# Kernel tuning notes

Hardware: AMD Instinct MI355X
Metric: run time of the kernel (lower is better)

Reference implementation:

```python
import jax, jax.numpy as jnp
import numpy as np

N = 500000      # active voxels
C_IN = 16       # input voxel feature dim
# encoder channels per stage: 32, 64, 128


def setup_inputs() -> dict:
    key = jax.random.key(0)
    ks = jax.random.split(key, 16)

    def w(k, i, o):
        return jax.random.normal(k, (i, o), dtype=jnp.float32) * (1.0 / np.sqrt(i))

    d = {}
    d['feat'] = jax.random.normal(ks[0], (N, C_IN), dtype=jnp.float32)
    d['coords'] = jax.random.randint(ks[1], (N, 4), 0, 1024, dtype=jnp.int32)
    d['W_in'] = w(ks[2], C_IN, 32)
    d['W_enc1'] = w(ks[3], 32, 32)
    d['W_enc2'] = w(ks[4], 32, 64)
    d['W_enc3'] = w(ks[5], 64, 128)
    d['W_lat1'] = w(ks[6], 32, 32)
    d['W_lat2'] = w(ks[7], 64, 64)
    d['W_lat3'] = w(ks[8], 128, 128)
    d['W_merge1'] = w(ks[9], 64, 32)    # merge: 2*C_i -> C_i
    d['W_merge2'] = w(ks[10], 128, 64)
    d['W_merge3'] = w(ks[11], 256, 128)
    d['W_up1'] = w(ks[12], 32, 32)      # upsample: C_i -> C_{i-1}
    d['W_up2'] = w(ks[13], 64, 32)
    d['W_up3'] = w(ks[14], 128, 64)
    return d


def _forward(feat, W_in, W_enc1, W_enc2, W_enc3, W_lat1, W_lat2, W_lat3,
             W_merge1, W_merge2, W_merge3, W_up1, W_up2, W_up3):
    relu = jax.nn.relu
    # conv_input + encoder (1x1 submanifold sparse convs == per-voxel matmul)
    x = relu(feat @ W_in)
    e1 = relu(x @ W_enc1)
    e2 = relu(e1 @ W_enc2)
    e3 = relu(e2 @ W_enc3)
    enc = [e1, e2, e3]
    lats = [W_lat1, W_lat2, W_lat3]
    mrgs = [W_merge1, W_merge2, W_merge3]
    ups = [W_up1, W_up2, W_up3]
    x = e3
    for i in (2, 1, 0):  # decoder stages stage_num..1
        lat = relu(enc[i] @ lats[i])                    # lateral_layer
        # cat0(x_bottom) + cat1(lat): identity-placement 1x1 convs == concat
        cat = jnp.concatenate([x, lat], axis=-1)        # [N, 2*C_i]
        merge = relu(cat @ mrgs[i])                     # merge_layer 2C->C
        red = cat.reshape(cat.shape[0], -1, 2).sum(-1)  # reduce_channel: fixed pairwise-sum conv
        x = relu((merge + red) @ ups[i])                # residual add + upsample_layer
    return x  # ret['voxel_feats']


def reference(feat, coords, W_in, W_enc1, W_enc2, W_enc3, W_lat1, W_lat2, W_lat3,
              W_merge1, W_merge2, W_merge3, W_up1, W_up2, W_up3):
    # coords define sparse structure; for 1x1 subm convs the math only touches features
    return _forward(feat, W_in, W_enc1, W_enc2, W_enc3, W_lat1, W_lat2, W_lat3,
                    W_merge1, W_merge2, W_merge3, W_up1, W_up2, W_up3)
```

## Files before the change

kernel.cpp:

```cpp
#include <hip/hip_runtime.h>

typedef unsigned short u16;
typedef _Float16 h16;
typedef __attribute__((ext_vector_type(8))) _Float16 half8;
typedef __attribute__((ext_vector_type(8))) unsigned short ushort8;
typedef __attribute__((ext_vector_type(4))) float f32x4;

#define N_STRIPS 31250
#define NPAIRS   15625
#define STRIP    16384

#define MFMA16(A,B,C) __builtin_amdgcn_mfma_f32_16x16x32_f16(A,B,C,0,0,0)

#define LBAR() asm volatile("s_waitcnt lgkmcnt(0)\n\ts_barrier" ::: "memory")

#define F_L0   0
#define F_L1   2
#define F_L2   4
#define F_L3   8
#define F_L4   24
#define F_L5   56
#define F_L6   120
#define F_L7   136
#define F_L8   144
#define F_L9   160
#define F_L10  164
#define F_L11  166
#define F_L12  170
#define NFRAG  172

__device__ __forceinline__ u16 hb(h16 h) { union { h16 h; u16 u; } v; v.h = h; return v.u; }

__global__ __launch_bounds__(256) void pack_w(
    const float* w0, const float* w1, const float* w2, const float* w3, const float* w4,
    const float* w5, const float* w6, const float* w7, const float* w8, const float* w9,
    const float* w10, const float* w11, const float* w12, u16* __restrict__ packed)
{
  const float* ws[13] = {w0,w1,w2,w3,w4,w5,w6,w7,w8,w9,w10,w11,w12};
  const int Ka[13]  = {16,32,32,64,128,256,128,64,128,64,32,64,32};
  const int KT[13]  = {1,1,1,2,4,8,4,2,4,2,1,2,1};
  const int CO[13]  = {32,32,64,128,128,128,64,64,64,32,32,32,32};
  const int FO[13]  = {F_L0,F_L1,F_L2,F_L3,F_L4,F_L5,F_L6,F_L7,F_L8,F_L9,F_L10,F_L11,F_L12};
  int g = blockIdx.x * 256 + threadIdx.x;
  int f = g >> 6, lane = g & 63;
  if (f >= NFRAG) return;
  int layer = 0;
#pragma unroll
  for (int i = 1; i < 13; ++i) if (f >= FO[i]) layer = i;
  int fl = f - FO[layer];
  int kt = fl % KT[layer];
  int ct = fl / KT[layer];
  int cout = CO[layer];
  int quad = lane >> 4;
  int col  = ct * 16 + (lane & 15);
  u16 thi[8], tlo[8];
#pragma unroll
  for (int j = 0; j < 8; ++j) {
    int k = kt * 32 + quad * 8 + j;
    float w = (k < Ka[layer]) ? ws[layer][k * cout + col] : 0.f;
    h16 h = (h16)w;
    h16 l = (h16)(w - (float)h);
    thi[j] = hb(h); tlo[j] = hb(l);
  }
  u16* dst = packed + ((size_t)f * 64 + lane) * 16;
  *(ushort8*)dst       = *(const ushort8*)thi;
  *(ushort8*)(dst + 8) = *(const ushort8*)tlo;
}


__device__ __forceinline__ void splitw(h16* dst, int idx, int lo, float v) {
  h16 h = (h16)v;
  dst[idx]      = h;
  dst[idx + lo] = (h16)(v - (float)h);
}
__device__ __forceinline__ float red4(const h16* cat, int cs, int rr, int cc) {
  const h16* p = cat + rr * cs + 2 * cc;
  const h16* q = p + 16 * cs;
  return (float)p[0] + (float)p[1] + (float)q[0] + (float)q[1];
}

template<int EPI>
__device__ __forceinline__ void epilogue(
    f32x4 a0, f32x4 a1, int ct, int lane,
    h16* dst, int ds, int colb, const h16* cat, int cs,
    float* __restrict__ gout, int row0)
{
  const int l15 = lane & 15, quad = lane >> 4;
  const int dlo = 16 * ds;
#pragma unroll
  for (int r = 0; r < 4; ++r) {
    const int rr = quad * 4 + r;
    const int cc = ct * 16 + l15;
    float v0 = a0[r] > 0.f ? a0[r] : 0.f;
    float v1 = a1[r] > 0.f ? a1[r] : 0.f;
    if (EPI == 1) {
      v0 += red4(cat, cs, rr, cc);
      v1 += red4(cat + STRIP, cs, rr, cc);
    }
    if (EPI <= 1) {
      splitw(dst,         rr * ds + colb + cc, dlo, v0);
      splitw(dst + STRIP, rr * ds + colb + cc, dlo, v1);
    } else {
      gout[(size_t)(row0 + rr) * 32 + cc]      = v0;
      gout[(size_t)(row0 + 16 + rr) * 32 + cc] = v1;
    }
  }
}

template<int KT, int EPI>
__device__ __forceinline__ void layerW(
    const h16* __restrict__ asrc, int as,
    const h16* __restrict__ wp, int foff, int ct, int lane,
    half8 pbh, half8 pbl,
    h16* dst, int ds, int colb, const h16* cat, int cs,
    float* __restrict__ gout, int row0)
{
  const int l15 = lane & 15, quad = lane >> 4;
  const int abase = l15 * as + quad * 8;
  const int alo = 16 * as;
  f32x4 a0 = {0.f,0.f,0.f,0.f}, a1 = {0.f,0.f,0.f,0.f};
#pragma unroll
  for (int kt = 0; kt < KT; ++kt) {
    half8 bhv, blv;
    if (kt == 0) { bhv = pbh; blv = pbl; }
    else {
      const h16* fp = wp + (((size_t)(foff + ct * KT + kt)) * 64 + lane) * 16;
      bhv = *(const half8*)fp;
      blv = *(const half8*)(fp + 8);
    }
    half8 ah0 = *(const half8*)(asrc + abase + kt * 32);
    half8 al0 = *(const half8*)(asrc + alo + abase + kt * 32);
    half8 ah1 = *(const half8*)(asrc + STRIP + abase + kt * 32);
    half8 al1 = *(const half8*)(asrc + STRIP + alo + abase + kt * 32);
    a0 = MFMA16(al0, bhv, a0); a0 = MFMA16(ah0, blv, a0); a0 = MFMA16(ah0, bhv, a0);
    a1 = MFMA16(al1, bhv, a1); a1 = MFMA16(ah1, blv, a1); a1 = MFMA16(ah1, bhv, a1);
  }
  epilogue<EPI>(a0, a1, ct, lane, dst, ds, colb, cat, cs, gout, row0);
}

#define PFB(FOFF, CT_, KT_)                                                       \
  do { const h16* _fp = wp + (((size_t)((FOFF) + (CT_) * (KT_))) * 64 + lane) * 16; \
       pbh = *(const half8*)_fp; pbl = *(const half8*)(_fp + 8); } while (0)

__global__ __launch_bounds__(512, 4) void backbone(
    const float* __restrict__ feat, const h16* __restrict__ wp, float* __restrict__ out)
{
  __shared__ h16 lds[2 * STRIP];
  const int lane = threadIdx.x & 63;
  const int wv   = threadIdx.x >> 6;
  const int l15 = lane & 15, quad = lane >> 4;
  const int row0 = blockIdx.x * 32;

  h16* E1 = lds;            const int SE1 = 40;
  h16* E2 = lds + 1280;     const int SE2 = 72;
  h16* CT = lds + 3584;     const int SCT = 264;
  h16* MR = lds + 12032;    const int SMR = 136;

  half8 pbh, pbl;

  if (wv < 2) {
    PFB(F_L0, wv, 1);
    h16 th0[8] = {0,0,0,0,0,0,0,0}, tl0[8] = {0,0,0,0,0,0,0,0};
    h16 th1[8] = {0,0,0,0,0,0,0,0}, tl1[8] = {0,0,0,0,0,0,0,0};
    if (quad < 2) {
      const float* s0 = feat + (size_t)(row0 + l15) * 16 + quad * 8;
      const float* s1 = feat + (size_t)(row0 + 16 + l15) * 16 + quad * 8;
#pragma unroll
      for (int j = 0; j < 8; ++j) {
        float v0 = s0[j], v1 = s1[j];
        h16 h0 = (h16)v0, h1 = (h16)v1;
        th0[j] = h0; tl0[j] = (h16)(v0 - (float)h0);
        th1[j] = h1; tl1[j] = (h16)(v1 - (float)h1);
      }
    }
    half8 ah0 = *(const half8*)th0, al0 = *(const half8*)tl0;
    half8 ah1 = *(const half8*)th1, al1 = *(const half8*)tl1;
    f32x4 a0 = {0.f,0.f,0.f,0.f}, a1 = {0.f,0.f,0.f,0.f};
    a0 = MFMA16(al0, pbh, a0); a0 = MFMA16(ah0, pbl, a0); a0 = MFMA16(ah0, pbh, a0);
    a1 = MFMA16(al1, pbh, a1); a1 = MFMA16(ah1, pbl, a1); a1 = MFMA16(ah1, pbh, a1);
    epilogue<0>(a0, a1, wv, lane, CT, SCT, 0, nullptr, 0, nullptr, 0);
    PFB(F_L1, wv, 1);
  }
  LBAR();

  if (wv < 2) {
    layerW<1,0>(CT,SCT, wp, F_L1, wv, lane, pbh,pbl, E1,SE1,0, nullptr,0, nullptr,0);
  }
  if (wv < 4) PFB(F_L2, wv, 1);
  LBAR();

  if (wv < 4) {
    layerW<1,0>(E1,SE1, wp, F_L2, wv, lane, pbh,pbl, E2,SE2,0, nullptr,0, nullptr,0);
  }
  PFB(F_L3, wv, 2);
  LBAR();

  layerW<2,0>(E2,SE2, wp, F_L3, wv, lane, pbh,pbl, CT,SCT,0, nullptr,0, nullptr,0);
  PFB(F_L4, wv, 4);
  LBAR();

  layerW<4,0>(CT,SCT, wp, F_L4, wv, lane, pbh,pbl, CT,SCT,128, nullptr,0, nullptr,0);
  PFB(F_L5, wv, 8);
  LBAR();

  layerW<8,1>(CT,SCT, wp, F_L5, wv, lane, pbh,pbl, MR,SMR,0, CT,SCT, nullptr,0);
  if (wv < 4) PFB(F_L6, wv, 4); else PFB(F_L7, wv - 4, 2);
  LBAR();

  if (wv < 4) {
    layerW<4,0>(MR,SMR, wp, F_L6, wv, lane, pbh,pbl, CT,SCT,0,  nullptr,0, nullptr,0);
  } else {
    layerW<2,0>(E2,SE2, wp, F_L7, wv - 4, lane, pbh,pbl, CT,SCT,64, nullptr,0, nullptr,0);
  }
  if (wv < 4) PFB(F_L8, wv, 4);
  LBAR();

  if (wv < 4) {
    layerW<4,1>(CT,SCT, wp, F_L8, wv, lane, pbh,pbl, MR,SMR,0, CT,SCT, nullptr,0);
  }
  if (wv < 2) PFB(F_L9, wv, 2);
  else if (wv < 4) PFB(F_L10, wv - 2, 1);
  LBAR();

  if (wv < 2) {
    layerW<2,0>(MR,SMR, wp, F_L9, wv, lane, pbh,pbl, CT,SCT,0,  nullptr,0, nullptr,0);
  } else if (wv < 4) {
    layerW<1,0>(E1,SE1, wp, F_L10, wv - 2, lane, pbh,pbl, CT,SCT,32, nullptr,0, nullptr,0);
  }
  if (wv < 2) PFB(F_L11, wv, 2);
  LBAR();

  if (wv < 2) {
    layerW<2,1>(CT,SCT, wp, F_L11, wv, lane, pbh,pbl, MR,SMR,0, CT,SCT, nullptr,0);
    PFB(F_L12, wv, 1);
  }
  LBAR();

  if (wv < 2) {
    layerW<1,2>(MR,SMR, wp, F_L12, wv, lane, pbh,pbl, nullptr,0,0, nullptr,0, out, row0);
  }
}

extern "C" void kernel_launch(void* const* d_in, const int* in_sizes, int n_in,
                              void* d_out, int out_size, void* d_ws, size_t ws_size,
                              hipStream_t stream) {
  (void)in_sizes; (void)n_in; (void)out_size; (void)ws_size;
  u16* packed = (u16*)d_ws;

  hipLaunchKernelGGL(pack_w, dim3(43), dim3(256), 0, stream,
      (const float*)d_in[2],  (const float*)d_in[3],  (const float*)d_in[4],
      (const float*)d_in[5],  (const float*)d_in[8],  (const float*)d_in[11],
      (const float*)d_in[14], (const float*)d_in[7],  (const float*)d_in[10],
      (const float*)d_in[13], (const float*)d_in[6],  (const float*)d_in[9],
      (const float*)d_in[12], packed);

  hipLaunchKernelGGL(backbone, dim3(NPAIRS), dim3(512), 0, stream,
                     (const float*)d_in[0], (const h16*)packed, (float*)d_out);
}
```

Measured before the change: 452.5 us.

## Process four 16-row strips per block with multi-tile waves to reuse weights

Each block now handles 64 voxels (four strips) in 128KB of dynamic LDS instead of 32, and waves are remapped so that each computes several column tiles and/or strips. Every weight fragment loaded from global memory is then reused across more MFMAs, and all 8 waves stay busy in the narrow layers instead of idling. The feature load is vectorised and a bounds check handles the tail block. In exchange, LDS per block grows fourfold and occupancy drops to two blocks per CU, while register pressure rises from the multi-accumulator tiles.

```diff
diff --git a/kernel.cpp b/kernel.cpp
--- a/kernel.cpp
+++ b/kernel.cpp
@@ -3,12 +3,22 @@
 typedef unsigned short u16;
 typedef _Float16 h16;
 typedef __attribute__((ext_vector_type(8))) _Float16 half8;
+typedef __attribute__((ext_vector_type(2))) _Float16 half2v;
 typedef __attribute__((ext_vector_type(8))) unsigned short ushort8;
 typedef __attribute__((ext_vector_type(4))) float f32x4;
 
-#define N_STRIPS 31250
-#define NPAIRS   15625
-#define STRIP    16384
+#define NVOX  500000
+#define NBLK  7813
+#define STRIP 16384
+
+#define AE1 0
+#define SE1 40
+#define AE2 1280
+#define SE2 72
+#define ACT 3584
+#define SCT 264
+#define AMR 12032
+#define SMR 136
 
 #define MFMA16(A,B,C) __builtin_amdgcn_mfma_f32_16x16x32_f16(A,B,C,0,0,0)
 
@@ -68,177 +78,192 @@
 }
 
 
-__device__ __forceinline__ void splitw(h16* dst, int idx, int lo, float v) {
-  h16 h = (h16)v;
-  dst[idx]      = h;
-  dst[idx + lo] = (h16)(v - (float)h);
-}
-__device__ __forceinline__ float red4(const h16* cat, int cs, int rr, int cc) {
-  const h16* p = cat + rr * cs + 2 * cc;
-  const h16* q = p + 16 * cs;
-  return (float)p[0] + (float)p[1] + (float)q[0] + (float)q[1];
-}
-
-template<int EPI>
-__device__ __forceinline__ void epilogue(
-    f32x4 a0, f32x4 a1, int ct, int lane,
-    h16* dst, int ds, int colb, const h16* cat, int cs,
+__device__ __forceinline__ float red2(const h16* p) {
+  half2v v = *reinterpret_cast<const half2v*>(p);
+  return (float)v.x + (float)v.y;
+}
+
+template<int KT, int NCT, int CTS, int NSP, int EPI>
+__device__ __forceinline__ void unitW(
+    h16* __restrict__ lds, int s0, int aoff, int as,
+    const h16* __restrict__ wp, int foff, int c0, int lane,
+    half8 pbh, half8 pbl,
+    int doff, int ds, int colb, int catoff, int cs,
     float* __restrict__ gout, int row0)
 {
   const int l15 = lane & 15, quad = lane >> 4;
-  const int dlo = 16 * ds;
-#pragma unroll
-  for (int r = 0; r < 4; ++r) {
-    const int rr = quad * 4 + r;
-    const int cc = ct * 16 + l15;
-    float v0 = a0[r] > 0.f ? a0[r] : 0.f;
-    float v1 = a1[r] > 0.f ? a1[r] : 0.f;
-    if (EPI == 1) {
-      v0 += red4(cat, cs, rr, cc);
-      v1 += red4(cat + STRIP, cs, rr, cc);
-    }
+  const int abase = aoff + l15 * as + quad * 8;
+  f32x4 acc[NSP][NCT];
+#pragma unroll
+  for (int sp = 0; sp < NSP; ++sp)
+#pragma unroll
+    for (int i = 0; i < NCT; ++i) acc[sp][i] = (f32x4){0.f,0.f,0.f,0.f};
+
+#pragma unroll
+  for (int kt = 0; kt < KT; ++kt) {
+    half8 bh[NCT], bl[NCT];
+#pragma unroll
+    for (int i = 0; i < NCT; ++i) {
+      if (kt == 0 && i == 0) { bh[0] = pbh; bl[0] = pbl; }
+      else {
+        const h16* fp = wp + (((size_t)(foff + (c0 + i * CTS) * KT + kt)) * 64 + lane) * 16;
+        bh[i] = *(const half8*)fp;
+        bl[i] = *(const half8*)(fp + 8);
+      }
+    }
+#pragma unroll
+    for (int sp = 0; sp < NSP; ++sp) {
+      const h16* ab = lds + (s0 + sp) * STRIP + abase + kt * 32;
+      half8 ah = *(const half8*)ab;
+      half8 al = *(const half8*)(ab + 16 * as);
+#pragma unroll
+      for (int i = 0; i < NCT; ++i) {
+        acc[sp][i] = MFMA16(al, bh[i], acc[sp][i]);
+        acc[sp][i] = MFMA16(ah, bl[i], acc[sp][i]);
+        acc[sp][i] = MFMA16(ah, bh[i], acc[sp][i]);
+      }
+    }
+  }
+
+#pragma unroll
+  for (int sp = 0; sp < NSP; ++sp) {
     if (EPI <= 1) {
-      splitw(dst,         rr * ds + colb + cc, dlo, v0);
-      splitw(dst + STRIP, rr * ds + colb + cc, dlo, v1);
+      h16* dstS = lds + (s0 + sp) * STRIP + doff;
+      const h16* catS = lds + (s0 + sp) * STRIP + catoff;
+      const int dlo = 16 * ds;
+#pragma unroll
+      for (int i = 0; i < NCT; ++i) {
+        const int cc = (c0 + i * CTS) * 16 + l15;
+#pragma unroll
+        for (int r = 0; r < 4; ++r) {
+          const int rr = quad * 4 + r;
+          float v = acc[sp][i][r];
+          v = v > 0.f ? v : 0.f;
+          if (EPI == 1)
+            v += red2(catS + rr * cs + 2 * cc) + red2(catS + (rr + 16) * cs + 2 * cc);
+          const int idx = rr * ds + colb + cc;
+          h16 h = (h16)v;
+          dstS[idx]       = h;
+          dstS[idx + dlo] = (h16)(v - (float)h);
+        }
+      }
     } else {
-      gout[(size_t)(row0 + rr) * 32 + cc]      = v0;
-      gout[(size_t)(row0 + 16 + rr) * 32 + cc] = v1;
-    }
-  }
-}
-
-template<int KT, int EPI>
-__device__ __forceinline__ void layerW(
-    const h16* __restrict__ asrc, int as,
-    const h16* __restrict__ wp, int foff, int ct, int lane,
-    half8 pbh, half8 pbl,
-    h16* dst, int ds, int colb, const h16* cat, int cs,
-    float* __restrict__ gout, int row0)
-{
-  const int l15 = lane & 15, quad = lane >> 4;
-  const int abase = l15 * as + quad * 8;
-  const int alo = 16 * as;
-  f32x4 a0 = {0.f,0.f,0.f,0.f}, a1 = {0.f,0.f,0.f,0.f};
-#pragma unroll
-  for (int kt = 0; kt < KT; ++kt) {
-    half8 bhv, blv;
-    if (kt == 0) { bhv = pbh; blv = pbl; }
-    else {
-      const h16* fp = wp + (((size_t)(foff + ct * KT + kt)) * 64 + lane) * 16;
-      bhv = *(const half8*)fp;
-      blv = *(const half8*)(fp + 8);
-    }
-    half8 ah0 = *(const half8*)(asrc + abase + kt * 32);
-    half8 al0 = *(const half8*)(asrc + alo + abase + kt * 32);
-    half8 ah1 = *(const half8*)(asrc + STRIP + abase + kt * 32);
-    half8 al1 = *(const half8*)(asrc + STRIP + alo + abase + kt * 32);
-    a0 = MFMA16(al0, bhv, a0); a0 = MFMA16(ah0, blv, a0); a0 = MFMA16(ah0, bhv, a0);
-    a1 = MFMA16(al1, bhv, a1); a1 = MFMA16(ah1, blv, a1); a1 = MFMA16(ah1, bhv, a1);
-  }
-  epilogue<EPI>(a0, a1, ct, lane, dst, ds, colb, cat, cs, gout, row0);
-}
-
-#define PFB(FOFF, CT_, KT_)                                                       \
-  do { const h16* _fp = wp + (((size_t)((FOFF) + (CT_) * (KT_))) * 64 + lane) * 16; \
+      const int gr0 = row0 + (s0 + sp) * 16;
+#pragma unroll
+      for (int i = 0; i < NCT; ++i) {
+        const int cc = (c0 + i * CTS) * 16 + l15;
+#pragma unroll
+        for (int r = 0; r < 4; ++r) {
+          const int rr = quad * 4 + r;
+          float v = acc[sp][i][r];
+          v = v > 0.f ? v : 0.f;
+          const int grow = gr0 + rr;
+          if (grow < NVOX) gout[(size_t)grow * 32 + cc] = v;
+        }
+      }
+    }
+  }
+}
+
+#define PFB(FOFF, CIDX, KT_)                                                        \
+  do { const h16* _fp = wp + (((size_t)((FOFF) + (CIDX) * (KT_))) * 64 + lane) * 16; \
        pbh = *(const half8*)_fp; pbl = *(const half8*)(_fp + 8); } while (0)
-
-__global__ __launch_bounds__(512, 4) void backbone(
+#define PFB2(FOFF, CIDX, KT_)                                                       \
+  do { const h16* _fp = wp + (((size_t)((FOFF) + (CIDX) * (KT_))) * 64 + lane) * 16; \
+       pbh2 = *(const half8*)_fp; pbl2 = *(const half8*)(_fp + 8); } while (0)
+
+__global__ __launch_bounds__(512, 2) void backbone(
     const float* __restrict__ feat, const h16* __restrict__ wp, float* __restrict__ out)
 {
-  __shared__ h16 lds[2 * STRIP];
+  extern __shared__ h16 lds[];
   const int lane = threadIdx.x & 63;
   const int wv   = threadIdx.x >> 6;
   const int l15 = lane & 15, quad = lane >> 4;
-  const int row0 = blockIdx.x * 32;
-
-  h16* E1 = lds;            const int SE1 = 40;
-  h16* E2 = lds + 1280;     const int SE2 = 72;
-  h16* CT = lds + 3584;     const int SCT = 264;
-  h16* MR = lds + 12032;    const int SMR = 136;
-
-  half8 pbh, pbl;
-
-  if (wv < 2) {
-    PFB(F_L0, wv, 1);
-    h16 th0[8] = {0,0,0,0,0,0,0,0}, tl0[8] = {0,0,0,0,0,0,0,0};
-    h16 th1[8] = {0,0,0,0,0,0,0,0}, tl1[8] = {0,0,0,0,0,0,0,0};
-    if (quad < 2) {
-      const float* s0 = feat + (size_t)(row0 + l15) * 16 + quad * 8;
-      const float* s1 = feat + (size_t)(row0 + 16 + l15) * 16 + quad * 8;
-#pragma unroll
-      for (int j = 0; j < 8; ++j) {
-        float v0 = s0[j], v1 = s1[j];
-        h16 h0 = (h16)v0, h1 = (h16)v1;
-        th0[j] = h0; tl0[j] = (h16)(v0 - (float)h0);
-        th1[j] = h1; tl1[j] = (h16)(v1 - (float)h1);
-      }
-    }
-    half8 ah0 = *(const half8*)th0, al0 = *(const half8*)tl0;
-    half8 ah1 = *(const half8*)th1, al1 = *(const half8*)tl1;
-    f32x4 a0 = {0.f,0.f,0.f,0.f}, a1 = {0.f,0.f,0.f,0.f};
-    a0 = MFMA16(al0, pbh, a0); a0 = MFMA16(ah0, pbl, a0); a0 = MFMA16(ah0, pbh, a0);
-    a1 = MFMA16(al1, pbh, a1); a1 = MFMA16(ah1, pbl, a1); a1 = MFMA16(ah1, pbh, a1);
-    epilogue<0>(a0, a1, wv, lane, CT, SCT, 0, nullptr, 0, nullptr, 0);
-    PFB(F_L1, wv, 1);
-  }
-  LBAR();
-
-  if (wv < 2) {
-    layerW<1,0>(CT,SCT, wp, F_L1, wv, lane, pbh,pbl, E1,SE1,0, nullptr,0, nullptr,0);
-  }
-  if (wv < 4) PFB(F_L2, wv, 1);
-  LBAR();
-
-  if (wv < 4) {
-    layerW<1,0>(E1,SE1, wp, F_L2, wv, lane, pbh,pbl, E2,SE2,0, nullptr,0, nullptr,0);
-  }
-  PFB(F_L3, wv, 2);
-  LBAR();
-
-  layerW<2,0>(E2,SE2, wp, F_L3, wv, lane, pbh,pbl, CT,SCT,0, nullptr,0, nullptr,0);
-  PFB(F_L4, wv, 4);
-  LBAR();
-
-  layerW<4,0>(CT,SCT, wp, F_L4, wv, lane, pbh,pbl, CT,SCT,128, nullptr,0, nullptr,0);
-  PFB(F_L5, wv, 8);
-  LBAR();
-
-  layerW<8,1>(CT,SCT, wp, F_L5, wv, lane, pbh,pbl, MR,SMR,0, CT,SCT, nullptr,0);
-  if (wv < 4) PFB(F_L6, wv, 4); else PFB(F_L7, wv - 4, 2);
-  LBAR();
-
-  if (wv < 4) {
-    layerW<4,0>(MR,SMR, wp, F_L6, wv, lane, pbh,pbl, CT,SCT,0,  nullptr,0, nullptr,0);
-  } else {
-    layerW<2,0>(E2,SE2, wp, F_L7, wv - 4, lane, pbh,pbl, CT,SCT,64, nullptr,0, nullptr,0);
-  }
-  if (wv < 4) PFB(F_L8, wv, 4);
-  LBAR();
-
-  if (wv < 4) {
-    layerW<4,1>(CT,SCT, wp, F_L8, wv, lane, pbh,pbl, MR,SMR,0, CT,SCT, nullptr,0);
-  }
-  if (wv < 2) PFB(F_L9, wv, 2);
-  else if (wv < 4) PFB(F_L10, wv - 2, 1);
-  LBAR();
-
-  if (wv < 2) {
-    layerW<2,0>(MR,SMR, wp, F_L9, wv, lane, pbh,pbl, CT,SCT,0,  nullptr,0, nullptr,0);
-  } else if (wv < 4) {
-    layerW<1,0>(E1,SE1, wp, F_L10, wv - 2, lane, pbh,pbl, CT,SCT,32, nullptr,0, nullptr,0);
-  }
-  if (wv < 2) PFB(F_L11, wv, 2);
-  LBAR();
-
-  if (wv < 2) {
-    layerW<2,1>(CT,SCT, wp, F_L11, wv, lane, pbh,pbl, MR,SMR,0, CT,SCT, nullptr,0);
-    PFB(F_L12, wv, 1);
-  }
-  LBAR();
-
-  if (wv < 2) {
-    layerW<1,2>(MR,SMR, wp, F_L12, wv, lane, pbh,pbl, nullptr,0,0, nullptr,0, out, row0);
-  }
+  const int row0 = blockIdx.x * 64;
+
+  const int sA = wv & 3;
+  const int cA = wv >> 2;
+  const int cB = wv & 3;
+  const int sB = (wv >> 2) * 2;
+
+  half8 pbh, pbl, pbh2, pbl2;
+
+  PFB(F_L0, cA, 1);
+  {
+    const int grow = row0 + sA * 16 + l15;
+    half8 ah = {0,0,0,0,0,0,0,0}, al = {0,0,0,0,0,0,0,0};
+    if (quad < 2 && grow < NVOX) {
+      const float* s = feat + (size_t)grow * 16 + quad * 8;
+      f32x4 u0 = *(const f32x4*)s;
+      f32x4 u1 = *(const f32x4*)(s + 4);
+      h16 th[8], tl[8];
+#pragma unroll
+      for (int j = 0; j < 4; ++j) {
+        h16 h = (h16)u0[j]; th[j] = h; tl[j] = (h16)(u0[j] - (float)h);
+      }
+#pragma unroll
+      for (int j = 0; j < 4; ++j) {
+        h16 h = (h16)u1[j]; th[4+j] = h; tl[4+j] = (h16)(u1[j] - (float)h);
+      }
+      ah = *(const half8*)th; al = *(const half8*)tl;
+    }
+    f32x4 a = {0.f,0.f,0.f,0.f};
+    a = MFMA16(al, pbh, a); a = MFMA16(ah, pbl, a); a = MFMA16(ah, pbh, a);
+    h16* dstS = lds + sA * STRIP + ACT;
+#pragma unroll
+    for (int r = 0; r < 4; ++r) {
+      const int rr = quad * 4 + r;
+      float v = a[r] > 0.f ? a[r] : 0.f;
+      const int idx = rr * SCT + cA * 16 + l15;
+      h16 h = (h16)v;
+      dstS[idx]            = h;
+      dstS[idx + 16 * SCT] = (h16)(v - (float)h);
+    }
+  }
+  PFB(F_L1, cA, 1);
+  LBAR();
+
+  unitW<1,1,1,1,0>(lds, sA, ACT, SCT, wp, F_L1, cA, lane, pbh, pbl, AE1, SE1, 0, 0, 0, nullptr, 0);
+  PFB(F_L2, cA, 1);
+  LBAR();
+
+  unitW<1,2,2,1,0>(lds, sA, AE1, SE1, wp, F_L2, cA, lane, pbh, pbl, AE2, SE2, 0, 0, 0, nullptr, 0);
+  PFB(F_L3, cB, 2);
+  LBAR();
+
+  unitW<2,2,4,2,0>(lds, sB, AE2, SE2, wp, F_L3, cB, lane, pbh, pbl, ACT, SCT, 0, 0, 0, nullptr, 0);
+  PFB(F_L4, cB, 4);
+  LBAR();
+
+  unitW<4,2,4,2,0>(lds, sB, ACT, SCT, wp, F_L4, cB, lane, pbh, pbl, ACT, SCT, 128, 0, 0, nullptr, 0);
+  PFB(F_L5, cB, 8);
+  LBAR();
+
+  unitW<8,2,4,2,1>(lds, sB, ACT, SCT, wp, F_L5, cB, lane, pbh, pbl, AMR, SMR, 0, ACT, SCT, nullptr, 0);
+  PFB (F_L6, cA, 4);
+  PFB2(F_L7, cA, 2);
+  LBAR();
+
+  unitW<4,2,2,1,0>(lds, sA, AMR, SMR, wp, F_L6, cA, lane, pbh,  pbl,  ACT, SCT, 0,  0, 0, nullptr, 0);
+  unitW<2,2,2,1,0>(lds, sA, AE2, SE2, wp, F_L7, cA, lane, pbh2, pbl2, ACT, SCT, 64, 0, 0, nullptr, 0);
+  PFB(F_L8, cA, 4);
+  LBAR();
+
+  unitW<4,2,2,1,1>(lds, sA, ACT, SCT, wp, F_L8, cA, lane, pbh, pbl, AMR, SMR, 0, ACT, SCT, nullptr, 0);
+  PFB (F_L9,  cA, 2);
+  PFB2(F_L10, cA, 1);
+  LBAR();
+
+  unitW<2,1,1,1,0>(lds, sA, AMR, SMR, wp, F_L9,  cA, lane, pbh,  pbl,  ACT, SCT, 0,  0, 0, nullptr, 0);
+  unitW<1,1,1,1,0>(lds, sA, AE1, SE1, wp, F_L10, cA, lane, pbh2, pbl2, ACT, SCT, 32, 0, 0, nullptr, 0);
+  PFB(F_L11, cA, 2);
+  LBAR();
+
+  unitW<2,1,1,1,1>(lds, sA, ACT, SCT, wp, F_L11, cA, lane, pbh, pbl, AMR, SMR, 0, ACT, SCT, nullptr, 0);
+  PFB(F_L12, cA, 1);
+  LBAR();
+
+  unitW<1,1,1,1,2>(lds, sA, AMR, SMR, wp, F_L12, cA, lane, pbh, pbl, 0, 0, 0, 0, 0, out, row0);
 }
 
 extern "C" void kernel_launch(void* const* d_in, const int* in_sizes, int n_in,
@@ -246,6 +271,13 @@
                               hipStream_t stream) {
   (void)in_sizes; (void)n_in; (void)out_size; (void)ws_size;
   u16* packed = (u16*)d_ws;
+
+  static bool att_set = false;
+  if (!att_set) {
+    hipFuncSetAttribute((const void*)backbone,
+                        hipFuncAttributeMaxDynamicSharedMemorySize, 131072);
+    att_set = true;
+  }
 
   hipLaunchKernelGGL(pack_w, dim3(43), dim3(256), 0, stream,
       (const float*)d_in[2],  (const float*)d_in[3],  (const float*)d_in[4],
@@ -254,6 +286,6 @@
       (const float*)d_in[13], (const float*)d_in[6],  (const float*)d_in[9],
       (const float*)d_in[12], packed);
 
-  hipLaunchKernelGGL(backbone, dim3(NPAIRS), dim3(512), 0, stream,
+  hipLaunchKernelGGL(backbone, dim3(NBLK), dim3(512), 131072, stream,
                      (const float*)d_in[0], (const h16*)packed, (float*)d_out);
 }
```

Result: slower. 504.4 us (+11.5%).

## Interleave hi/lo fp16 pairs in LDS and alias merge buffer to shrink shared memory

Applied to the files above, without the earlier changes.

Activations in LDS are now stored with each value's hi and lo fp16 halves interleaved in one 32-bit word, replacing separate hi and lo planes. The MR buffer now overlaps CT, made safe by an extra barrier inside the layer-5 epilogue, which is placed after the reads of CT and before the writes. Together these shrink per-block LDS so the launch bound can rise to 6 blocks per CU. Operand loads now need shuffles to de-interleave, and the input load is vectorized. The intent is higher occupancy and fewer LDS store instructions, at the cost of extra shuffle ALU work and a possibly more fragile buffer-aliasing schedule.

```diff
diff --git a/kernel.cpp b/kernel.cpp
--- a/kernel.cpp
+++ b/kernel.cpp
@@ -1,14 +1,24 @@
 #include <hip/hip_runtime.h>
 
 typedef unsigned short u16;
+typedef unsigned int u32;
 typedef _Float16 h16;
+typedef __attribute__((ext_vector_type(4))) _Float16 half4;
 typedef __attribute__((ext_vector_type(8))) _Float16 half8;
 typedef __attribute__((ext_vector_type(8))) unsigned short ushort8;
 typedef __attribute__((ext_vector_type(4))) float f32x4;
 
-#define N_STRIPS 31250
-#define NPAIRS   15625
-#define STRIP    16384
+#define NPAIRS 15625
+#define STRIPO 11648
+
+#define AE1 0
+#define SE1 72
+#define AE2 1152
+#define SE2 136
+#define ACT 3328
+#define SCT 520
+#define AMR 3584
+#define SMR 520
 
 #define MFMA16(A,B,C) __builtin_amdgcn_mfma_f32_16x16x32_f16(A,B,C,0,0,0)
 
@@ -68,46 +78,20 @@
 }
 
 
-__device__ __forceinline__ void splitw(h16* dst, int idx, int lo, float v) {
+__device__ __forceinline__ void packw(h16* dst, int idx2, float v) {
   h16 h = (h16)v;
-  dst[idx]      = h;
-  dst[idx + lo] = (h16)(v - (float)h);
-}
-__device__ __forceinline__ float red4(const h16* cat, int cs, int rr, int cc) {
-  const h16* p = cat + rr * cs + 2 * cc;
-  const h16* q = p + 16 * cs;
-  return (float)p[0] + (float)p[1] + (float)q[0] + (float)q[1];
-}
-
-template<int EPI>
-__device__ __forceinline__ void epilogue(
-    f32x4 a0, f32x4 a1, int ct, int lane,
-    h16* dst, int ds, int colb, const h16* cat, int cs,
-    float* __restrict__ gout, int row0)
-{
-  const int l15 = lane & 15, quad = lane >> 4;
-  const int dlo = 16 * ds;
-#pragma unroll
-  for (int r = 0; r < 4; ++r) {
-    const int rr = quad * 4 + r;
-    const int cc = ct * 16 + l15;
-    float v0 = a0[r] > 0.f ? a0[r] : 0.f;
-    float v1 = a1[r] > 0.f ? a1[r] : 0.f;
-    if (EPI == 1) {
-      v0 += red4(cat, cs, rr, cc);
-      v1 += red4(cat + STRIP, cs, rr, cc);
-    }
-    if (EPI <= 1) {
-      splitw(dst,         rr * ds + colb + cc, dlo, v0);
-      splitw(dst + STRIP, rr * ds + colb + cc, dlo, v1);
-    } else {
-      gout[(size_t)(row0 + rr) * 32 + cc]      = v0;
-      gout[(size_t)(row0 + 16 + rr) * 32 + cc] = v1;
-    }
-  }
-}
-
-template<int KT, int EPI>
+  h16 l = (h16)(v - (float)h);
+  union { u16 s[2]; u32 u; } z;
+  z.s[0] = hb(h); z.s[1] = hb(l);
+  *reinterpret_cast<u32*>(dst + idx2) = z.u;
+}
+
+__device__ __forceinline__ float red2i(const h16* cat, int cs, int rr, int cc) {
+  half4 v = *reinterpret_cast<const half4*>(cat + rr * cs + 4 * cc);
+  return (float)v.x + (float)v.y + (float)v.z + (float)v.w;
+}
+
+template<int KT, int EPI, int BAR>
 __device__ __forceinline__ void layerW(
     const h16* __restrict__ asrc, int as,
     const h16* __restrict__ wp, int foff, int ct, int lane,
@@ -116,8 +100,7 @@
     float* __restrict__ gout, int row0)
 {
   const int l15 = lane & 15, quad = lane >> 4;
-  const int abase = l15 * as + quad * 8;
-  const int alo = 16 * as;
+  const int abase = l15 * as + quad * 16;
   f32x4 a0 = {0.f,0.f,0.f,0.f}, a1 = {0.f,0.f,0.f,0.f};
 #pragma unroll
   for (int kt = 0; kt < KT; ++kt) {
@@ -128,33 +111,66 @@
       bhv = *(const half8*)fp;
       blv = *(const half8*)(fp + 8);
     }
-    half8 ah0 = *(const half8*)(asrc + abase + kt * 32);
-    half8 al0 = *(const half8*)(asrc + alo + abase + kt * 32);
-    half8 ah1 = *(const half8*)(asrc + STRIP + abase + kt * 32);
-    half8 al1 = *(const half8*)(asrc + STRIP + alo + abase + kt * 32);
+    const h16* p0 = asrc + abase + kt * 64;
+    const h16* p1 = p0 + STRIPO;
+    half8 q0a = *(const half8*)p0, q0b = *(const half8*)(p0 + 8);
+    half8 q1a = *(const half8*)p1, q1b = *(const half8*)(p1 + 8);
+    half8 ah0 = __builtin_shufflevector(q0a, q0b, 0,2,4,6,8,10,12,14);
+    half8 al0 = __builtin_shufflevector(q0a, q0b, 1,3,5,7,9,11,13,15);
+    half8 ah1 = __builtin_shufflevector(q1a, q1b, 0,2,4,6,8,10,12,14);
+    half8 al1 = __builtin_shufflevector(q1a, q1b, 1,3,5,7,9,11,13,15);
     a0 = MFMA16(al0, bhv, a0); a0 = MFMA16(ah0, blv, a0); a0 = MFMA16(ah0, bhv, a0);
     a1 = MFMA16(al1, bhv, a1); a1 = MFMA16(ah1, blv, a1); a1 = MFMA16(ah1, bhv, a1);
   }
-  epilogue<EPI>(a0, a1, ct, lane, dst, ds, colb, cat, cs, gout, row0);
-}
-
-#define PFB(FOFF, CT_, KT_)                                                       \
-  do { const h16* _fp = wp + (((size_t)((FOFF) + (CT_) * (KT_))) * 64 + lane) * 16; \
+  const int cc = ct * 16 + l15;
+  float v0r[4], v1r[4];
+#pragma unroll
+  for (int r = 0; r < 4; ++r) {
+    const int rr = quad * 4 + r;
+    float v0 = a0[r] > 0.f ? a0[r] : 0.f;
+    float v1 = a1[r] > 0.f ? a1[r] : 0.f;
+    if (EPI == 1) {
+      v0 += red2i(cat, cs, rr, cc);
+      v1 += red2i(cat + STRIPO, cs, rr, cc);
+    }
+    v0r[r] = v0; v1r[r] = v1;
+  }
+  if (BAR) LBAR();
+  if (EPI <= 1) {
+#pragma unroll
+    for (int r = 0; r < 4; ++r) {
+      const int rr = quad * 4 + r;
+      const int idx2 = rr * ds + 2 * (colb + cc);
+      packw(dst, idx2, v0r[r]);
+      packw(dst + STRIPO, idx2, v1r[r]);
+    }
+  } else {
+#pragma unroll
+    for (int r = 0; r < 4; ++r) {
+      const int rr = quad * 4 + r;
+      gout[(size_t)(row0 + rr) * 32 + cc]      = v0r[r];
+      gout[(size_t)(row0 + 16 + rr) * 32 + cc] = v1r[r];
+    }
+  }
+}
+
+#define PFB(FOFF, CIDX, KT_)                                                        \
+  do { const h16* _fp = wp + (((size_t)((FOFF) + (CIDX) * (KT_))) * 64 + lane) * 16; \
        pbh = *(const half8*)_fp; pbl = *(const half8*)(_fp + 8); } while (0)
 
-__global__ __launch_bounds__(512, 4) void backbone(
+__global__ __launch_bounds__(512, 6) void backbone(
     const float* __restrict__ feat, const h16* __restrict__ wp, float* __restrict__ out)
 {
-  __shared__ h16 lds[2 * STRIP];
+  __shared__ h16 lds[2 * STRIPO];
   const int lane = threadIdx.x & 63;
   const int wv   = threadIdx.x >> 6;
   const int l15 = lane & 15, quad = lane >> 4;
   const int row0 = blockIdx.x * 32;
 
-  h16* E1 = lds;            const int SE1 = 40;
-  h16* E2 = lds + 1280;     const int SE2 = 72;
-  h16* CT = lds + 3584;     const int SCT = 264;
-  h16* MR = lds + 12032;    const int SMR = 136;
+  h16* E1 = lds + AE1;
+  h16* E2 = lds + AE2;
+  h16* CT = lds + ACT;
+  h16* MR = lds + AMR;
 
   half8 pbh, pbl;
 
@@ -165,12 +181,15 @@
     if (quad < 2) {
       const float* s0 = feat + (size_t)(row0 + l15) * 16 + quad * 8;
       const float* s1 = feat + (size_t)(row0 + 16 + l15) * 16 + quad * 8;
-#pragma unroll
-      for (int j = 0; j < 8; ++j) {
-        float v0 = s0[j], v1 = s1[j];
-        h16 h0 = (h16)v0, h1 = (h16)v1;
-        th0[j] = h0; tl0[j] = (h16)(v0 - (float)h0);
-        th1[j] = h1; tl1[j] = (h16)(v1 - (float)h1);
+      f32x4 u0a = *(const f32x4*)s0, u0b = *(const f32x4*)(s0 + 4);
+      f32x4 u1a = *(const f32x4*)s1, u1b = *(const f32x4*)(s1 + 4);
+#pragma unroll
+      for (int j = 0; j < 4; ++j) {
+        h16 h;
+        h = (h16)u0a[j]; th0[j]   = h; tl0[j]   = (h16)(u0a[j] - (float)h);
+        h = (h16)u0b[j]; th0[4+j] = h; tl0[4+j] = (h16)(u0b[j] - (float)h);
+        h = (h16)u1a[j]; th1[j]   = h; tl1[j]   = (h16)(u1a[j] - (float)h);
+        h = (h16)u1b[j]; th1[4+j] = h; tl1[4+j] = (h16)(u1b[j] - (float)h);
       }
     }
     half8 ah0 = *(const half8*)th0, al0 = *(const half8*)tl0;
@@ -178,66 +197,72 @@
     f32x4 a0 = {0.f,0.f,0.f,0.f}, a1 = {0.f,0.f,0.f,0.f};
     a0 = MFMA16(al0, pbh, a0); a0 = MFMA16(ah0, pbl, a0); a0 = MFMA16(ah0, pbh, a0);
     a1 = MFMA16(al1, pbh, a1); a1 = MFMA16(ah1, pbl, a1); a1 = MFMA16(ah1, pbh, a1);
-    epilogue<0>(a0, a1, wv, lane, CT, SCT, 0, nullptr, 0, nullptr, 0);
+#pragma unroll
+    for (int r = 0; r < 4; ++r) {
+      const int rr = quad * 4 + r;
+      const int idx2 = rr * SCT + 2 * (wv * 16 + l15);
+      packw(CT,          idx2, a0[r] > 0.f ? a0[r] : 0.f);
+      packw(CT + STRIPO, idx2, a1[r] > 0.f ? a1[r] : 0.f);
+    }
     PFB(F_L1, wv, 1);
   }
   LBAR();
 
   if (wv < 2) {
-    layerW<1,0>(CT,SCT, wp, F_L1, wv, lane, pbh,pbl, E1,SE1,0, nullptr,0, nullptr,0);
+    layerW<1,0,0>(CT,SCT, wp, F_L1, wv, lane, pbh,pbl, E1,SE1,0, nullptr,0, nullptr,0);
   }
   if (wv < 4) PFB(F_L2, wv, 1);
   LBAR();
 
   if (wv < 4) {
-    layerW<1,0>(E1,SE1, wp, F_L2, wv, lane, pbh,pbl, E2,SE2,0, nullptr,0, nullptr,0);
+    layerW<1,0,0>(E1,SE1, wp, F_L2, wv, lane, pbh,pbl, E2,SE2,0, nullptr,0, nullptr,0);
   }
   PFB(F_L3, wv, 2);
   LBAR();
 
-  layerW<2,0>(E2,SE2, wp, F_L3, wv, lane, pbh,pbl, CT,SCT,0, nullptr,0, nullptr,0);
+  layerW<2,0,0>(E2,SE2, wp, F_L3, wv, lane, pbh,pbl, CT,SCT,0, nullptr,0, nullptr,0);
   PFB(F_L4, wv, 4);
   LBAR();
 
-  layerW<4,0>(CT,SCT, wp, F_L4, wv, lane, pbh,pbl, CT,SCT,128, nullptr,0, nullptr,0);
+  layerW<4,0,0>(CT,SCT, wp, F_L4, wv, lane, pbh,pbl, CT,SCT,128, nullptr,0, nullptr,0);
   PFB(F_L5, wv, 8);
   LBAR();
 
-  layerW<8,1>(CT,SCT, wp, F_L5, wv, lane, pbh,pbl, MR,SMR,0, CT,SCT, nullptr,0);
+  layerW<8,1,1>(CT,SCT, wp, F_L5, wv, lane, pbh,pbl, MR,SMR,0, CT,SCT, nullptr,0);
   if (wv < 4) PFB(F_L6, wv, 4); else PFB(F_L7, wv - 4, 2);
   LBAR();
 
   if (wv < 4) {
-    layerW<4,0>(MR,SMR, wp, F_L6, wv, lane, pbh,pbl, CT,SCT,0,  nullptr,0, nullptr,0);
+    layerW<4,0,0>(MR,SMR, wp, F_L6, wv, lane, pbh,pbl, CT,SCT,0,  nullptr,0, nullptr,0);
   } else {
-    layerW<2,0>(E2,SE2, wp, F_L7, wv - 4, lane, pbh,pbl, CT,SCT,64, nullptr,0, nullptr,0);
+    layerW<2,0,0>(E2,SE2, wp, F_L7, wv - 4, lane, pbh,pbl, CT,SCT,64, nullptr,0, nullptr,0);
   }
   if (wv < 4) PFB(F_L8, wv, 4);
   LBAR();
 
   if (wv < 4) {
-    layerW<4,1>(CT,SCT, wp, F_L8, wv, lane, pbh,pbl, MR,SMR,0, CT,SCT, nullptr,0);
+    layerW<4,1,0>(CT,SCT, wp, F_L8, wv, lane, pbh,pbl, MR,SMR,0, CT,SCT, nullptr,0);
   }
   if (wv < 2) PFB(F_L9, wv, 2);
   else if (wv < 4) PFB(F_L10, wv - 2, 1);
   LBAR();
 
   if (wv < 2) {
-    layerW<2,0>(MR,SMR, wp, F_L9, wv, lane, pbh,pbl, CT,SCT,0,  nullptr,0, nullptr,0);
+    layerW<2,0,0>(MR,SMR, wp, F_L9, wv, lane, pbh,pbl, CT,SCT,0,  nullptr,0, nullptr,0);
   } else if (wv < 4) {
-    layerW<1,0>(E1,SE1, wp, F_L10, wv - 2, lane, pbh,pbl, CT,SCT,32, nullptr,0, nullptr,0);
+    layerW<1,0,0>(E1,SE1, wp, F_L10, wv - 2, lane, pbh,pbl, CT,SCT,32, nullptr,0, nullptr,0);
   }
   if (wv < 2) PFB(F_L11, wv, 2);
   LBAR();
 
   if (wv < 2) {
-    layerW<2,1>(CT,SCT, wp, F_L11, wv, lane, pbh,pbl, MR,SMR,0, CT,SCT, nullptr,0);
+    layerW<2,1,0>(CT,SCT, wp, F_L11, wv, lane, pbh,pbl, MR,SMR,0, CT,SCT, nullptr,0);
     PFB(F_L12, wv, 1);
   }
   LBAR();
 
   if (wv < 2) {
-    layerW<1,2>(MR,SMR, wp, F_L12, wv, lane, pbh,pbl, nullptr,0,0, nullptr,0, out, row0);
+    layerW<1,2,0>(MR,SMR, wp, F_L12, wv, lane, pbh,pbl, nullptr,0,0, nullptr,0, out, row0);
   }
 }
 
```

After: 449.1 us. About the same (-0.8%).
